# Kernel tuning notes

Hardware: AMD Instinct MI355X
Metric: run time of the kernel (lower is better)

The kernel has to match this reference:

```python
import jax, jax.numpy as jnp
import numpy as np

NUM_HEADS = 8

def _l2norm(t, eps=1e-12):
    # F.normalize(p=2, dim=-1) with eps clamp
    n = jnp.sqrt(jnp.sum(t * t, axis=-1, keepdims=True))
    return t / jnp.maximum(n, eps)

def setup_inputs() -> dict:
    key = jax.random.key(0)
    ks = jax.random.split(key, 4)
    B, N, C = 16, 3136, 768
    x = jax.random.normal(ks[0], (B, N, C), dtype=jnp.float32)
    W_qkv = jax.random.normal(ks[1], (C, 3 * C), dtype=jnp.float32) * (1.0 / np.sqrt(C))
    temp = jnp.ones((NUM_HEADS, 1, 1), dtype=jnp.float32)
    W_proj = jax.random.normal(ks[2], (C, C), dtype=jnp.float32) * (1.0 / np.sqrt(C))
    b_proj = jnp.zeros((C,), dtype=jnp.float32)
    return {"x": x, "W_qkv": W_qkv, "temp": temp, "W_proj": W_proj, "b_proj": b_proj}

def reference(x, W_qkv, temp, W_proj, b_proj):
    B, N, C = x.shape
    h = NUM_HEADS
    d = C // h
    qkv = (x @ W_qkv).reshape(B, N, 3, h, d)
    qkv = jnp.transpose(qkv, (2, 0, 3, 1, 4))  # [3,B,h,N,d]
    q, k, v = qkv[0], qkv[1], qkv[2]           # [B,h,N,d]
    # transpose to channel-major: [B,h,d,N]
    q = jnp.swapaxes(q, -2, -1)
    k = jnp.swapaxes(k, -2, -1)
    v = jnp.swapaxes(v, -2, -1)
    q = _l2norm(q)
    k = _l2norm(k)
    # attn = k @ q^T over token dim: [B,h,d,d]
    attn = jnp.einsum('bhcn,bhen->bhce', k, q)
    attn = attn * temp  # temp broadcasts [h,1,1]
    attn = jax.nn.softmax(attn, axis=-1)
    out = jnp.einsum('bhce,bhen->bhcn', attn, v)  # [B,h,d,N]
    out = jnp.transpose(out, (0, 3, 1, 2)).reshape(B, N, C)
    return out @ W_proj + b_proj
```

## Files before the change

kernel.cpp:

```cpp
#include <hip/hip_runtime.h>

using bf16x8 = __attribute__((ext_vector_type(8))) __bf16;
using f32x4  = __attribute__((ext_vector_type(4))) float;

#define AS1 __attribute__((address_space(1)))
#define AS3 __attribute__((address_space(3)))

#define SB()     __builtin_amdgcn_s_barrier()
#define LGKM0()  asm volatile("s_waitcnt lgkmcnt(0)")
#define VM0()    asm volatile("s_waitcnt vmcnt(0)")
#define SCHED0() __builtin_amdgcn_sched_barrier(0)

__device__ __forceinline__ unsigned short f2bf(float f) {
    unsigned int x = __float_as_uint(f);
    x += 0x7fffu + ((x >> 16) & 1u);
    return (unsigned short)(x >> 16);
}

__device__ __forceinline__ int xcd_remap(int orig, int nwg) {
    int q = nwg >> 3, r = nwg & 7;
    int xcd = orig & 7, lin = orig >> 3;
    return (xcd < r ? xcd * (q + 1) : r * (q + 1) + (xcd - r) * q) + lin;
}

__global__ void cvt_f32_bf16_kernel(const float4* __restrict__ in, ushort4* __restrict__ out, int n4) {
    int stride = gridDim.x * blockDim.x;
    for (int i = blockIdx.x * blockDim.x + threadIdx.x; i < n4; i += stride) {
        float4 v = in[i];
        ushort4 o;
        o.x = f2bf(v.x); o.y = f2bf(v.y); o.z = f2bf(v.z); o.w = f2bf(v.w);
        out[i] = o;
    }
}

__global__ void transpose_f32_bf16_kernel(const float* __restrict__ W, unsigned short* __restrict__ Wt,
                                          int K, int N) {
    __shared__ float tile[32][33];
    int n0 = blockIdx.x << 5, k0 = blockIdx.y << 5;
    int tx = threadIdx.x, ty = threadIdx.y;
#pragma unroll
    for (int i = 0; i < 32; i += 8)
        tile[ty + i][tx] = W[(size_t)(k0 + ty + i) * N + (n0 + tx)];
    __syncthreads();
#pragma unroll
    for (int i = 0; i < 32; i += 8)
        Wt[(size_t)(n0 + ty + i) * K + (k0 + tx)] = f2bf(tile[tx][ty + i]);
}

__device__ __forceinline__ bf16x8 lds_read_swz(const char* base, int row, int ks, int lane) {
    int kbyte = (ks << 6) + ((lane >> 4) << 4);
    int off = (row << 7) + (kbyte ^ ((row & 7) << 4));
    return *(const bf16x8*)(base + off);
}

__device__ __forceinline__ void stage256x64(const unsigned short* g, int ldaE, int Mcap,
                                            char* dst, int tid) {
#pragma unroll
    for (int r = 0; r < 4; ++r) {
        int i = (r << 9) + tid;
        int row = i >> 3, slot = i & 7;
        int rg = row < Mcap ? row : Mcap - 1;
        size_t srcb = (size_t)rg * ((size_t)ldaE << 1) + ((slot ^ (row & 7)) << 4);
        __builtin_amdgcn_global_load_lds(
            (AS1 unsigned int*)(unsigned long long)((const char*)g + srcb),
            (AS3 unsigned int*)(dst + (i << 4)), 16, 0, 0);
    }
}

template <int OUTMODE>
__global__ __launch_bounds__(512, 2)
void gemm256_8ph(const unsigned short* __restrict__ A, const unsigned short* __restrict__ Bt,
                 unsigned short* __restrict__ obf, float* __restrict__ of32,
                 const float* __restrict__ bias,
                 int K, int lda, int Nld, int nbx, int nmt, int Mrows,
                 long strideA, long strideB, long strideO) {
    __shared__ char smem[131072];
    int tid = threadIdx.x, lane = tid & 63, w = tid >> 6;
    int wm = w >> 2, wn = w & 3;
    int l15 = lane & 15;

    int wg = xcd_remap(blockIdx.x, gridDim.x);
    int bx = wg % nbx; int r1 = wg / nbx; int mt = r1 % nmt; int b = r1 / nmt;
    int m0 = mt << 8, n0 = bx << 8;
    int Mcap = Mrows - m0; if (Mcap > 256) Mcap = 256;
    const unsigned short* Ag = A + (long)b * strideA + (size_t)m0 * lda;
    const unsigned short* Bg = Bt + (long)b * strideB + (size_t)n0 * K;
    int nkt = K >> 6;

    f32x4 zz = {0.f, 0.f, 0.f, 0.f};
    f32x4 acc[8][4];
#pragma unroll
    for (int a = 0; a < 8; ++a)
#pragma unroll
        for (int c = 0; c < 4; ++c) acc[a][c] = zz;

    stage256x64(Ag, lda, Mcap, smem, tid);
    stage256x64(Bg, K, 256, smem + 32768, tid);
    VM0();
    SB(); SCHED0();

    for (int t = 0; t < nkt; ++t) {
        const char* Ab = smem + ((t & 1) << 16);
        const char* Bb = Ab + 32768;
        char* An = smem + (((t + 1) & 1) << 16);
        int arow = (wm << 7) + l15;
        int brow = (wn << 6) + l15;

        bf16x8 aF[4], aG[4], bL[4], bH[4];
#pragma unroll
        for (int f = 0; f < 4; ++f) aF[f] = lds_read_swz(Ab, arow + (f << 4), 0, lane);
#pragma unroll
        for (int f = 0; f < 4; ++f) bL[f] = lds_read_swz(Bb, brow + (f << 4), 0, lane);
        if (t + 1 < nkt) stage256x64(Ag + ((t + 1) << 6), lda, Mcap, An, tid);
        SB(); LGKM0(); SCHED0();
        __builtin_amdgcn_s_setprio(1);
#pragma unroll
        for (int fm = 0; fm < 4; ++fm)
#pragma unroll
            for (int fn = 0; fn < 4; ++fn)
                acc[fm][fn] = __builtin_amdgcn_mfma_f32_16x16x32_bf16(aF[fm], bL[fn], acc[fm][fn], 0, 0, 0);
        __builtin_amdgcn_s_setprio(0);
        SB(); SCHED0();
#pragma unroll
        for (int f = 0; f < 4; ++f) aG[f] = lds_read_swz(Ab, arow + 64 + (f << 4), 0, lane);
        if (t + 1 < nkt) stage256x64(Bg + ((t + 1) << 6), K, 256, An + 32768, tid);
        SB(); LGKM0(); SCHED0();
        __builtin_amdgcn_s_setprio(1);
#pragma unroll
        for (int fm = 0; fm < 4; ++fm)
#pragma unroll
            for (int fn = 0; fn < 4; ++fn)
                acc[fm + 4][fn] = __builtin_amdgcn_mfma_f32_16x16x32_bf16(aG[fm], bL[fn], acc[fm + 4][fn], 0, 0, 0);
        __builtin_amdgcn_s_setprio(0);
        SB(); SCHED0();
#pragma unroll
        for (int f = 0; f < 4; ++f) aF[f] = lds_read_swz(Ab, arow + (f << 4), 1, lane);
#pragma unroll
        for (int f = 0; f < 4; ++f) bH[f] = lds_read_swz(Bb, brow + (f << 4), 1, lane);
        SB(); LGKM0(); SCHED0();
        __builtin_amdgcn_s_setprio(1);
#pragma unroll
        for (int fm = 0; fm < 4; ++fm)
#pragma unroll
            for (int fn = 0; fn < 4; ++fn)
                acc[fm][fn] = __builtin_amdgcn_mfma_f32_16x16x32_bf16(aF[fm], bH[fn], acc[fm][fn], 0, 0, 0);
        __builtin_amdgcn_s_setprio(0);
        SB(); SCHED0();
#pragma unroll
        for (int f = 0; f < 4; ++f) aG[f] = lds_read_swz(Ab, arow + 64 + (f << 4), 1, lane);
        SB(); LGKM0(); SCHED0();
        __builtin_amdgcn_s_setprio(1);
#pragma unroll
        for (int fm = 0; fm < 4; ++fm)
#pragma unroll
            for (int fn = 0; fn < 4; ++fn)
                acc[fm + 4][fn] = __builtin_amdgcn_mfma_f32_16x16x32_bf16(aG[fm], bH[fn], acc[fm + 4][fn], 0, 0, 0);
        __builtin_amdgcn_s_setprio(0);
        if (t + 1 < nkt) VM0();
        SB(); SCHED0();
    }

    int rbase = m0 + (wm << 7) + ((lane >> 4) << 2);
    int cbase = n0 + (wn << 6) + l15;
    if (OUTMODE == 0) {
#pragma unroll
        for (int fm = 0; fm < 8; ++fm)
#pragma unroll
            for (int j = 0; j < 4; ++j) {
                size_t ro = (size_t)(rbase + (fm << 4) + j) * Nld;
#pragma unroll
                for (int fn = 0; fn < 4; ++fn)
                    obf[ro + cbase + (fn << 4)] = f2bf(acc[fm][fn][j]);
            }
    } else {
        float bv[4];
#pragma unroll
        for (int fn = 0; fn < 4; ++fn) bv[fn] = bias[cbase + (fn << 4)];
#pragma unroll
        for (int fm = 0; fm < 8; ++fm)
#pragma unroll
            for (int j = 0; j < 4; ++j) {
                int rr = rbase + (fm << 4) + j;
                if (rr < Mrows) {
                    size_t ro = (long)b * strideO + (size_t)rr * Nld;
#pragma unroll
                    for (int fn = 0; fn < 4; ++fn)
                        of32[ro + cbase + (fn << 4)] = acc[fm][fn][j] + bv[fn];
                }
            }
    }
}

__global__ __launch_bounds__(256)
void cov_mfma_kernel(const unsigned short* __restrict__ qkv, float* __restrict__ S,
                     float* __restrict__ qn2, float* __restrict__ kn2) {
    __shared__ unsigned short Kl[96 * 40];
    __shared__ unsigned short Ql[96 * 40];
    int bh = blockIdx.x;
    int b = bh >> 3, h = bh & 7;
    int tok0 = blockIdx.y * 448;
    int tid = threadIdx.x;
    int lane = tid & 63, w = tid >> 6;
    int wr = w & 1, wc = w >> 1;
    int rot = tid & 7;

    f32x4 zz = {0.f, 0.f, 0.f, 0.f};
    f32x4 acc[3][3];
#pragma unroll
    for (int a = 0; a < 3; ++a)
#pragma unroll
        for (int c = 0; c < 3; ++c) acc[a][c] = zz;
    float qn = 0.f, kn = 0.f;

    const uint4* qg = (const uint4*)qkv;

    for (int step = 0; step < 14; ++step) {
        int tokBase = b * 3136 + tok0 + (step << 5);
        __syncthreads();
#pragma unroll
        for (int r = 0; r < 3; ++r) {
            int idx = (r << 8) + tid;
            int isK = idx >= 384;
            int j = isK ? idx - 384 : idx;
            int tok = j / 12, c = j % 12;
            uint4 u = qg[(size_t)(tokBase + tok) * 288 + h * 12 + (isK ? 96 : 0) + c];
            unsigned short* dst = isK ? Kl : Ql;
            const unsigned short* us = (const unsigned short*)&u;
#pragma unroll
            for (int i = 0; i < 8; ++i) {
                int e = (i + rot) & 7;
                dst[(c * 8 + e) * 40 + tok] = us[e];
            }
        }
        __syncthreads();
        if (tid < 96) {
#pragma unroll
            for (int t = 0; t < 4; ++t) {
                bf16x8 v = *(const bf16x8*)((const char*)Ql + tid * 80 + (t << 4));
#pragma unroll
                for (int i = 0; i < 8; ++i) { float f = (float)v[i]; qn = fmaf(f, f, qn); }
            }
        } else if (tid >= 128 && tid < 224) {
            int c = tid - 128;
#pragma unroll
            for (int t = 0; t < 4; ++t) {
                bf16x8 v = *(const bf16x8*)((const char*)Kl + c * 80 + (t << 4));
#pragma unroll
                for (int i = 0; i < 8; ++i) { float f = (float)v[i]; kn = fmaf(f, f, kn); }
            }
        }
        int kbyte = (lane >> 4) << 4;
        bf16x8 af[3], bfv[3];
#pragma unroll
        for (int f = 0; f < 3; ++f)
            af[f] = *(const bf16x8*)((const char*)Kl + (wr * 48 + f * 16 + (lane & 15)) * 80 + kbyte);
#pragma unroll
        for (int f = 0; f < 3; ++f)
            bfv[f] = *(const bf16x8*)((const char*)Ql + (wc * 48 + f * 16 + (lane & 15)) * 80 + kbyte);
#pragma unroll
        for (int fm = 0; fm < 3; ++fm)
#pragma unroll
            for (int fn = 0; fn < 3; ++fn)
                acc[fm][fn] = __builtin_amdgcn_mfma_f32_16x16x32_bf16(af[fm], bfv[fn], acc[fm][fn], 0, 0, 0);
    }

    float* Sb = S + (size_t)bh * 9216;
    int rloc = wr * 48 + ((lane >> 4) << 2);
    int cloc = wc * 48 + (lane & 15);
#pragma unroll
    for (int fm = 0; fm < 3; ++fm)
#pragma unroll
        for (int fn = 0; fn < 3; ++fn)
#pragma unroll
            for (int j = 0; j < 4; ++j)
                atomicAdd(&Sb[(rloc + fm * 16 + j) * 96 + cloc + fn * 16], acc[fm][fn][j]);
    if (tid < 96) atomicAdd(&qn2[bh * 96 + tid], qn);
    if (tid >= 128 && tid < 224) atomicAdd(&kn2[bh * 96 + tid - 128], kn);
}

__global__ __launch_bounds__(128)
void softmax_kernel(const float* __restrict__ S, const float* __restrict__ qn2,
                    const float* __restrict__ kn2, const float* __restrict__ temp,
                    unsigned short* __restrict__ attnT) {
    int bh = blockIdx.x, h = bh & 7;
    __shared__ float Sl[96 * 97];
    __shared__ float qinv[96];
    int tid = threadIdx.x;
    const float* Sg = S + (size_t)bh * 9216;
    for (int i = tid; i < 9216; i += 128) Sl[(i / 96) * 97 + (i % 96)] = Sg[i];
    if (tid < 96) qinv[tid] = 1.f / fmaxf(sqrtf(qn2[bh * 96 + tid]), 1e-12f);
    __syncthreads();
    if (tid < 96) {
        int c = tid;
        float scale = (1.f / fmaxf(sqrtf(kn2[bh * 96 + c]), 1e-12f)) * temp[h];
        float* row = &Sl[c * 97];
        float mx = -3.4e38f;
        for (int e = 0; e < 96; ++e) {
            float v = row[e] * scale * qinv[e];
            row[e] = v;
            mx = fmaxf(mx, v);
        }
        float s = 0.f;
        for (int e = 0; e < 96; ++e) {
            float p = __expf(row[e] - mx);
            row[e] = p;
            s += p;
        }
        float inv = 1.f / s;
        unsigned short* ab = attnT + (size_t)bh * 9216;
        for (int e = 0; e < 96; ++e) ab[e * 96 + c] = f2bf(row[e] * inv);
    }
}

__global__ __launch_bounds__(256)
void attn_M_kernel(const unsigned short* __restrict__ attnT, const unsigned short* __restrict__ wprojt,
                   unsigned short* __restrict__ MT) {
    int bh = blockIdx.x >> 2, oc = blockIdx.x & 3;
    int b = bh >> 3, h = bh & 7;
    int tid = threadIdx.x, lane = tid & 63, w = tid >> 6;
    int o0 = oc * 192 + w * 48;
    const unsigned short* At = attnT + (size_t)bh * 9216;

    f32x4 zz = {0.f, 0.f, 0.f, 0.f};
    f32x4 acc[6][3];
#pragma unroll
    for (int f = 0; f < 6; ++f)
#pragma unroll
        for (int g = 0; g < 3; ++g) acc[f][g] = zz;

#pragma unroll
    for (int ks = 0; ks < 3; ++ks) {
        int koff = ks * 32 + ((lane >> 4) << 3);
        bf16x8 a[6], bb[3];
#pragma unroll
        for (int f = 0; f < 6; ++f)
            a[f] = *(const bf16x8*)(At + (size_t)(f * 16 + (lane & 15)) * 96 + koff);
#pragma unroll
        for (int g = 0; g < 3; ++g)
            bb[g] = *(const bf16x8*)(wprojt + (size_t)(o0 + g * 16 + (lane & 15)) * 768 + h * 96 + koff);
#pragma unroll
        for (int f = 0; f < 6; ++f)
#pragma unroll
            for (int g = 0; g < 3; ++g)
                acc[f][g] = __builtin_amdgcn_mfma_f32_16x16x32_bf16(a[f], bb[g], acc[f][g], 0, 0, 0);
    }

#pragma unroll
    for (int f = 0; f < 6; ++f)
#pragma unroll
        for (int g = 0; g < 3; ++g) {
            int e = f * 16 + ((lane >> 4) << 2);
            int o = o0 + g * 16 + (lane & 15);
            ushort4 pk;
            pk.x = f2bf(acc[f][g][0]); pk.y = f2bf(acc[f][g][1]);
            pk.z = f2bf(acc[f][g][2]); pk.w = f2bf(acc[f][g][3]);
            *(ushort4*)&MT[((size_t)b * 768 + o) * 768 + h * 96 + e] = pk;
        }
}

extern "C" void kernel_launch(void* const* d_in, const int* in_sizes, int n_in,
                              void* d_out, int out_size, void* d_ws, size_t ws_size,
                              hipStream_t stream) {
    const float* x     = (const float*)d_in[0];
    const float* Wqkv  = (const float*)d_in[1];
    const float* temp  = (const float*)d_in[2];
    const float* Wproj = (const float*)d_in[3];
    const float* bproj = (const float*)d_in[4];
    float* out = (float*)d_out;
    char* ws = (char*)d_ws;

    unsigned short* xbf    = (unsigned short*)(ws);
    unsigned short* qkvbf  = (unsigned short*)(ws + 77070336);
    unsigned short* wqkvt  = (unsigned short*)(ws + 308281344);
    unsigned short* wprojt = (unsigned short*)(ws + 311820288);
    float*          Sbuf   = (float*)        (ws + 312999936);
    float*          qn2    = (float*)        (ws + 317718528);
    float*          kn2    = (float*)        (ws + 317767680);
    unsigned short* attnT  = (unsigned short*)(ws + 317816832);
    unsigned short* MT     = xbf;

    hipMemsetAsync(Sbuf, 0, 4718592 + 49152 + 49152, stream);

    cvt_f32_bf16_kernel<<<2048, 256, 0, stream>>>((const float4*)x, (ushort4*)xbf, 38535168 / 4);
    transpose_f32_bf16_kernel<<<dim3(72, 24), dim3(32, 8), 0, stream>>>(Wqkv, wqkvt, 768, 2304);
    transpose_f32_bf16_kernel<<<dim3(24, 24), dim3(32, 8), 0, stream>>>(Wproj, wprojt, 768, 768);

    gemm256_8ph<0><<<196 * 9, 512, 0, stream>>>(xbf, wqkvt, qkvbf, nullptr, nullptr,
                                                768, 768, 2304, 9, 196, 50176, 0, 0, 0);
    cov_mfma_kernel<<<dim3(128, 7), 256, 0, stream>>>(qkvbf, Sbuf, qn2, kn2);
    softmax_kernel<<<128, 128, 0, stream>>>(Sbuf, qn2, kn2, temp, attnT);
    attn_M_kernel<<<512, 256, 0, stream>>>(attnT, wprojt, MT);
    gemm256_8ph<1><<<16 * 13 * 3, 512, 0, stream>>>(qkvbf + 1536, MT, nullptr, out, bproj,
                                                    768, 2304, 768, 3, 13, 3136,
                                                    7225344L, 589824L, 2408448L);
}
```

Before: 431.2 us.

## Switch GEMMs to 256x128 tiles with triple-buffered LDS and counted vmcnt waits

Both GEMMs move from 256x256 tiles with double buffering to 256x128 tiles with a three-stage LDS ring. Loads run two k-steps ahead and use a partial vmcnt wait, so global loads overlap compute instead of draining every iteration. The smaller tile doubles the grid and halves the per-wave accumulators. In exchange, B reuse per tile drops, A is loaded twice as often, and 144KB of LDS per block may limit occupancy to one block per CU despite the launch bounds of 2.

```diff
diff --git a/kernel.cpp b/kernel.cpp
--- a/kernel.cpp
+++ b/kernel.cpp
@@ -9,6 +9,7 @@
 #define SB()     __builtin_amdgcn_s_barrier()
 #define LGKM0()  asm volatile("s_waitcnt lgkmcnt(0)")
 #define VM0()    asm volatile("s_waitcnt vmcnt(0)")
+#define VM6()    asm volatile("s_waitcnt vmcnt(6)")
 #define SCHED0() __builtin_amdgcn_sched_barrier(0)
 
 __device__ __forceinline__ unsigned short f2bf(float f) {
@@ -53,8 +54,8 @@
     return *(const bf16x8*)(base + off);
 }
 
-__device__ __forceinline__ void stage256x64(const unsigned short* g, int ldaE, int Mcap,
-                                            char* dst, int tid) {
+__device__ __forceinline__ void stageA256(const unsigned short* g, int ldaE, int Mcap,
+                                          char* dst, int tid) {
 #pragma unroll
     for (int r = 0; r < 4; ++r) {
         int i = (r << 9) + tid;
@@ -66,105 +67,103 @@
             (AS3 unsigned int*)(dst + (i << 4)), 16, 0, 0);
     }
 }
+__device__ __forceinline__ void stageB128(const unsigned short* g, int ldbE, char* dst, int tid) {
+#pragma unroll
+    for (int r = 0; r < 2; ++r) {
+        int i = (r << 9) + tid;
+        int row = i >> 3, slot = i & 7;
+        size_t srcb = (size_t)row * ((size_t)ldbE << 1) + ((slot ^ (row & 7)) << 4);
+        __builtin_amdgcn_global_load_lds(
+            (AS1 unsigned int*)(unsigned long long)((const char*)g + srcb),
+            (AS3 unsigned int*)(dst + (i << 4)), 16, 0, 0);
+    }
+}
 
 template <int OUTMODE>
 __global__ __launch_bounds__(512, 2)
-void gemm256_8ph(const unsigned short* __restrict__ A, const unsigned short* __restrict__ Bt,
-                 unsigned short* __restrict__ obf, float* __restrict__ of32,
-                 const float* __restrict__ bias,
-                 int K, int lda, int Nld, int nbx, int nmt, int Mrows,
-                 long strideA, long strideB, long strideO) {
-    __shared__ char smem[131072];
+void gemm_cnt_kernel(const unsigned short* __restrict__ A, const unsigned short* __restrict__ Bt,
+                     unsigned short* __restrict__ obf, float* __restrict__ of32,
+                     const float* __restrict__ bias,
+                     int K, int lda, int Nld, int nbx, int nmt, int Mrows,
+                     long strideA, long strideB, long strideO) {
+    __shared__ char smem[147456];
     int tid = threadIdx.x, lane = tid & 63, w = tid >> 6;
-    int wm = w >> 2, wn = w & 3;
+    int wm = w >> 1, wn = w & 1;
     int l15 = lane & 15;
 
     int wg = xcd_remap(blockIdx.x, gridDim.x);
     int bx = wg % nbx; int r1 = wg / nbx; int mt = r1 % nmt; int b = r1 / nmt;
-    int m0 = mt << 8, n0 = bx << 8;
+    int m0 = mt << 8, n0 = bx << 7;
     int Mcap = Mrows - m0; if (Mcap > 256) Mcap = 256;
     const unsigned short* Ag = A + (long)b * strideA + (size_t)m0 * lda;
     const unsigned short* Bg = Bt + (long)b * strideB + (size_t)n0 * K;
     int nkt = K >> 6;
 
     f32x4 zz = {0.f, 0.f, 0.f, 0.f};
-    f32x4 acc[8][4];
-#pragma unroll
-    for (int a = 0; a < 8; ++a)
+    f32x4 acc[4][4];
+#pragma unroll
+    for (int a = 0; a < 4; ++a)
 #pragma unroll
         for (int c = 0; c < 4; ++c) acc[a][c] = zz;
 
-    stage256x64(Ag, lda, Mcap, smem, tid);
-    stage256x64(Bg, K, 256, smem + 32768, tid);
-    VM0();
+    stageA256(Ag, lda, Mcap, smem, tid);
+    stageB128(Bg, K, smem + 98304, tid);
+    if (nkt > 1) {
+        stageA256(Ag + 64, lda, Mcap, smem + 32768, tid);
+        stageB128(Bg + 64, K, smem + 98304 + 16384, tid);
+        VM6();
+    } else {
+        VM0();
+    }
     SB(); SCHED0();
 
+    int arow = (wm << 6) + l15;
+    int brow = (wn << 6) + l15;
+
     for (int t = 0; t < nkt; ++t) {
-        const char* Ab = smem + ((t & 1) << 16);
-        const char* Bb = Ab + 32768;
-        char* An = smem + (((t + 1) & 1) << 16);
-        int arow = (wm << 7) + l15;
-        int brow = (wn << 6) + l15;
-
-        bf16x8 aF[4], aG[4], bL[4], bH[4];
+        const char* Ab = smem + (t % 3) * 32768;
+        const char* Bb = smem + 98304 + (t % 3) * 16384;
+        char* An = smem + ((t + 2) % 3) * 32768;
+        char* Bn = smem + 98304 + ((t + 2) % 3) * 16384;
+
+        bf16x8 aF[4], bF[4];
 #pragma unroll
         for (int f = 0; f < 4; ++f) aF[f] = lds_read_swz(Ab, arow + (f << 4), 0, lane);
 #pragma unroll
-        for (int f = 0; f < 4; ++f) bL[f] = lds_read_swz(Bb, brow + (f << 4), 0, lane);
-        if (t + 1 < nkt) stage256x64(Ag + ((t + 1) << 6), lda, Mcap, An, tid);
+        for (int f = 0; f < 4; ++f) bF[f] = lds_read_swz(Bb, brow + (f << 4), 0, lane);
+        if (t + 2 < nkt) stageA256(Ag + ((t + 2) << 6), lda, Mcap, An, tid);
         SB(); LGKM0(); SCHED0();
         __builtin_amdgcn_s_setprio(1);
 #pragma unroll
         for (int fm = 0; fm < 4; ++fm)
 #pragma unroll
             for (int fn = 0; fn < 4; ++fn)
-                acc[fm][fn] = __builtin_amdgcn_mfma_f32_16x16x32_bf16(aF[fm], bL[fn], acc[fm][fn], 0, 0, 0);
+                acc[fm][fn] = __builtin_amdgcn_mfma_f32_16x16x32_bf16(aF[fm], bF[fn], acc[fm][fn], 0, 0, 0);
         __builtin_amdgcn_s_setprio(0);
         SB(); SCHED0();
 #pragma unroll
-        for (int f = 0; f < 4; ++f) aG[f] = lds_read_swz(Ab, arow + 64 + (f << 4), 0, lane);
-        if (t + 1 < nkt) stage256x64(Bg + ((t + 1) << 6), K, 256, An + 32768, tid);
+        for (int f = 0; f < 4; ++f) aF[f] = lds_read_swz(Ab, arow + (f << 4), 1, lane);
+#pragma unroll
+        for (int f = 0; f < 4; ++f) bF[f] = lds_read_swz(Bb, brow + (f << 4), 1, lane);
+        if (t + 2 < nkt) stageB128(Bg + ((t + 2) << 6), K, Bn, tid);
         SB(); LGKM0(); SCHED0();
         __builtin_amdgcn_s_setprio(1);
 #pragma unroll
         for (int fm = 0; fm < 4; ++fm)
 #pragma unroll
             for (int fn = 0; fn < 4; ++fn)
-                acc[fm + 4][fn] = __builtin_amdgcn_mfma_f32_16x16x32_bf16(aG[fm], bL[fn], acc[fm + 4][fn], 0, 0, 0);
+                acc[fm][fn] = __builtin_amdgcn_mfma_f32_16x16x32_bf16(aF[fm], bF[fn], acc[fm][fn], 0, 0, 0);
         __builtin_amdgcn_s_setprio(0);
+        if (t + 2 < nkt) VM6();
+        else if (t + 1 < nkt) VM0();
         SB(); SCHED0();
-#pragma unroll
-        for (int f = 0; f < 4; ++f) aF[f] = lds_read_swz(Ab, arow + (f << 4), 1, lane);
-#pragma unroll
-        for (int f = 0; f < 4; ++f) bH[f] = lds_read_swz(Bb, brow + (f << 4), 1, lane);
-        SB(); LGKM0(); SCHED0();
-        __builtin_amdgcn_s_setprio(1);
-#pragma unroll
-        for (int fm = 0; fm < 4; ++fm)
-#pragma unroll
-            for (int fn = 0; fn < 4; ++fn)
-                acc[fm][fn] = __builtin_amdgcn_mfma_f32_16x16x32_bf16(aF[fm], bH[fn], acc[fm][fn], 0, 0, 0);
-        __builtin_amdgcn_s_setprio(0);
-        SB(); SCHED0();
-#pragma unroll
-        for (int f = 0; f < 4; ++f) aG[f] = lds_read_swz(Ab, arow + 64 + (f << 4), 1, lane);
-        SB(); LGKM0(); SCHED0();
-        __builtin_amdgcn_s_setprio(1);
-#pragma unroll
-        for (int fm = 0; fm < 4; ++fm)
-#pragma unroll
-            for (int fn = 0; fn < 4; ++fn)
-                acc[fm + 4][fn] = __builtin_amdgcn_mfma_f32_16x16x32_bf16(aG[fm], bH[fn], acc[fm + 4][fn], 0, 0, 0);
-        __builtin_amdgcn_s_setprio(0);
-        if (t + 1 < nkt) VM0();
-        SB(); SCHED0();
-    }
-
-    int rbase = m0 + (wm << 7) + ((lane >> 4) << 2);
+    }
+
+    int rbase = m0 + (wm << 6) + ((lane >> 4) << 2);
     int cbase = n0 + (wn << 6) + l15;
     if (OUTMODE == 0) {
 #pragma unroll
-        for (int fm = 0; fm < 8; ++fm)
+        for (int fm = 0; fm < 4; ++fm)
 #pragma unroll
             for (int j = 0; j < 4; ++j) {
                 size_t ro = (size_t)(rbase + (fm << 4) + j) * Nld;
@@ -177,7 +176,7 @@
 #pragma unroll
         for (int fn = 0; fn < 4; ++fn) bv[fn] = bias[cbase + (fn << 4)];
 #pragma unroll
-        for (int fm = 0; fm < 8; ++fm)
+        for (int fm = 0; fm < 4; ++fm)
 #pragma unroll
             for (int j = 0; j < 4; ++j) {
                 int rr = rbase + (fm << 4) + j;
@@ -385,12 +384,12 @@
     transpose_f32_bf16_kernel<<<dim3(72, 24), dim3(32, 8), 0, stream>>>(Wqkv, wqkvt, 768, 2304);
     transpose_f32_bf16_kernel<<<dim3(24, 24), dim3(32, 8), 0, stream>>>(Wproj, wprojt, 768, 768);
 
-    gemm256_8ph<0><<<196 * 9, 512, 0, stream>>>(xbf, wqkvt, qkvbf, nullptr, nullptr,
-                                                768, 768, 2304, 9, 196, 50176, 0, 0, 0);
+    gemm_cnt_kernel<0><<<196 * 18, 512, 0, stream>>>(xbf, wqkvt, qkvbf, nullptr, nullptr,
+                                                     768, 768, 2304, 18, 196, 50176, 0, 0, 0);
     cov_mfma_kernel<<<dim3(128, 7), 256, 0, stream>>>(qkvbf, Sbuf, qn2, kn2);
     softmax_kernel<<<128, 128, 0, stream>>>(Sbuf, qn2, kn2, temp, attnT);
     attn_M_kernel<<<512, 256, 0, stream>>>(attnT, wprojt, MT);
-    gemm256_8ph<1><<<16 * 13 * 3, 512, 0, stream>>>(qkvbf + 1536, MT, nullptr, out, bproj,
-                                                    768, 2304, 768, 3, 13, 3136,
-                                                    7225344L, 589824L, 2408448L);
-}
+    gemm_cnt_kernel<1><<<16 * 13 * 6, 512, 0, stream>>>(qkvbf + 1536, MT, nullptr, out, bproj,
+                                                        768, 2304, 768, 6, 13, 3136,
+                                                        7225344L, 589824L, 2408448L);
+}
```

After: 457.9 us. 6.2% more time.

## Restage GEMM pipeline in half tiles and fuse prep and softmax kernels

Applied to the files above, without the earlier changes.

The bf16 GEMM now stages A and B tiles as 128-row and 64-row halves, with two K-steps per loop iteration. Each half's global-to-LDS load is issued between MFMA clusters, and a partial vmcnt wait lets loads stay in flight across barriers. The launch bound drops to one block per CU, and the bf16 output uses nontemporal stores. The input conversion, both weight transposes and the memset are merged into one prep kernel. Softmax is fused with the attn×Wproj kernel through LDS, which removes the attnT round trip and several launches, at the cost of computing each softmax four times.

```diff
diff --git a/kernel.cpp b/kernel.cpp
--- a/kernel.cpp
+++ b/kernel.cpp
@@ -7,9 +7,10 @@
 #define AS3 __attribute__((address_space(3)))
 
 #define SB()     __builtin_amdgcn_s_barrier()
+#define SCHED0() __builtin_amdgcn_sched_barrier(0)
 #define LGKM0()  asm volatile("s_waitcnt lgkmcnt(0)")
+#define VM6()    asm volatile("s_waitcnt vmcnt(6)")
 #define VM0()    asm volatile("s_waitcnt vmcnt(0)")
-#define SCHED0() __builtin_amdgcn_sched_barrier(0)
 
 __device__ __forceinline__ unsigned short f2bf(float f) {
     unsigned int x = __float_as_uint(f);
@@ -23,57 +24,102 @@
     return (xcd < r ? xcd * (q + 1) : r * (q + 1) + (xcd - r) * q) + lin;
 }
 
-__global__ void cvt_f32_bf16_kernel(const float4* __restrict__ in, ushort4* __restrict__ out, int n4) {
-    int stride = gridDim.x * blockDim.x;
-    for (int i = blockIdx.x * blockDim.x + threadIdx.x; i < n4; i += stride) {
-        float4 v = in[i];
-        ushort4 o;
-        o.x = f2bf(v.x); o.y = f2bf(v.y); o.z = f2bf(v.z); o.w = f2bf(v.w);
-        out[i] = o;
-    }
-}
-
-__global__ void transpose_f32_bf16_kernel(const float* __restrict__ W, unsigned short* __restrict__ Wt,
-                                          int K, int N) {
+__global__ __launch_bounds__(256)
+void prep_kernel(const float* __restrict__ x, ushort4* __restrict__ xbf,
+                 const float* __restrict__ Wqkv, unsigned short* __restrict__ wqkvt,
+                 const float* __restrict__ Wproj, unsigned short* __restrict__ wprojt,
+                 float4* __restrict__ zbase) {
     __shared__ float tile[32][33];
-    int n0 = blockIdx.x << 5, k0 = blockIdx.y << 5;
-    int tx = threadIdx.x, ty = threadIdx.y;
-#pragma unroll
-    for (int i = 0; i < 32; i += 8)
-        tile[ty + i][tx] = W[(size_t)(k0 + ty + i) * N + (n0 + tx)];
-    __syncthreads();
-#pragma unroll
-    for (int i = 0; i < 32; i += 8)
-        Wt[(size_t)(n0 + ty + i) * K + (k0 + tx)] = f2bf(tile[tx][ty + i]);
-}
-
-__device__ __forceinline__ bf16x8 lds_read_swz(const char* base, int row, int ks, int lane) {
-    int kbyte = (ks << 6) + ((lane >> 4) << 4);
-    int off = (row << 7) + (kbyte ^ ((row & 7) << 4));
-    return *(const bf16x8*)(base + off);
-}
-
-__device__ __forceinline__ void stage256x64(const unsigned short* g, int ldaE, int Mcap,
-                                            char* dst, int tid) {
-#pragma unroll
-    for (int r = 0; r < 4; ++r) {
+    int bid = blockIdx.x, tid = threadIdx.x;
+    if (bid < 2304) {
+        const float* W; unsigned short* Wt; int K = 768, N; int bx, by;
+        if (bid < 1728) { W = Wqkv; Wt = wqkvt; N = 2304; bx = bid % 72; by = bid / 72; }
+        else            { int t = bid - 1728; W = Wproj; Wt = wprojt; N = 768; bx = t % 24; by = t / 24; }
+        int n0 = bx << 5, k0 = by << 5;
+        int tx = tid & 31, ty = tid >> 5;
+#pragma unroll
+        for (int i = 0; i < 32; i += 8)
+            tile[ty + i][tx] = W[(size_t)(k0 + ty + i) * N + (n0 + tx)];
+        __syncthreads();
+#pragma unroll
+        for (int i = 0; i < 32; i += 8)
+            Wt[(size_t)(n0 + ty + i) * K + (k0 + tx)] = f2bf(tile[tx][ty + i]);
+    } else if (bid < 4352) {
+        int vb = bid - 2304;
+        const float4* in = (const float4*)x;
+        int n4 = 38535168 / 4;
+        int stride = 2048 * 256;
+        for (int i = vb * 256 + tid; i < n4; i += stride) {
+            float4 v = in[i];
+            ushort4 o;
+            o.x = f2bf(v.x); o.y = f2bf(v.y); o.z = f2bf(v.z); o.w = f2bf(v.w);
+            xbf[i] = o;
+        }
+    } else {
+        int z = bid - 4352;
+        float4 zz4 = {0.f, 0.f, 0.f, 0.f};
+        for (int i = z * 256 + tid; i < 301056; i += 294 * 256) zbase[i] = zz4;
+    }
+}
+
+__device__ __forceinline__ void stA8(const char* Asrc, int ldaB, int Mcap, int h,
+                                     char* dst, int tid) {
+#pragma unroll
+    for (int r = 0; r < 2; ++r) {
         int i = (r << 9) + tid;
-        int row = i >> 3, slot = i & 7;
-        int rg = row < Mcap ? row : Mcap - 1;
-        size_t srcb = (size_t)rg * ((size_t)ldaE << 1) + ((slot ^ (row & 7)) << 4);
+        int rho = i >> 3, s = i & 7;
+        int grow = ((rho >> 6) << 7) + (h << 6) + (rho & 63);
+        if (grow >= Mcap) grow = Mcap - 1;
         __builtin_amdgcn_global_load_lds(
-            (AS1 unsigned int*)(unsigned long long)((const char*)g + srcb),
+            (AS1 unsigned int*)(unsigned long long)(Asrc + (size_t)grow * ldaB + ((s ^ (rho & 7)) << 4)),
             (AS3 unsigned int*)(dst + (i << 4)), 16, 0, 0);
     }
 }
+__device__ __forceinline__ void stB8(const char* Bsrc, int ldbB, int h, char* dst, int tid) {
+#pragma unroll
+    for (int r = 0; r < 2; ++r) {
+        int i = (r << 9) + tid;
+        int rho = i >> 3, s = i & 7;
+        int grow = ((rho >> 5) << 6) + (h << 5) + (rho & 31);
+        __builtin_amdgcn_global_lds:
+        __builtin_amdgcn_global_load_lds(
+            (AS1 unsigned int*)(unsigned long long)(Bsrc + (size_t)grow * ldbB + ((s ^ (rho & 7)) << 4)),
+            (AS3 unsigned int*)(dst + (i << 4)), 16, 0, 0);
+    }
+}
+
+__device__ __forceinline__ bf16x8 rdA8(const char* smem, int buf, int rh, int wm,
+                                       int f, int ks, int lane) {
+    int rho = (wm << 6) + (f << 4) + (lane & 15);
+    int kb = ((ks << 2) + (lane >> 4)) << 4;
+    return *(const bf16x8*)(smem + (buf << 16) + (rh << 14) + rho * 128 + (kb ^ ((rho & 7) << 4)));
+}
+__device__ __forceinline__ bf16x8 rdB8(const char* smem, int buf, int ch, int wn,
+                                       int g, int ks, int lane) {
+    int rho = (wn << 5) + (g << 4) + (lane & 15);
+    int kb = ((ks << 2) + (lane >> 4)) << 4;
+    return *(const bf16x8*)(smem + (buf << 16) + 32768 + (ch << 14) + rho * 128 + (kb ^ ((rho & 7) << 4)));
+}
+
+#define CL16(MB, CB, BREG)                                                     \
+    __builtin_amdgcn_s_setprio(1);                                             \
+    _Pragma("unroll") for (int f_ = 0; f_ < 4; ++f_) {                         \
+        _Pragma("unroll") for (int g_ = 0; g_ < 2; ++g_) {                     \
+            acc[(MB) + f_][(CB) + g_] = __builtin_amdgcn_mfma_f32_16x16x32_bf16( \
+                aF[f_][0], BREG[g_][0], acc[(MB) + f_][(CB) + g_], 0, 0, 0);   \
+            acc[(MB) + f_][(CB) + g_] = __builtin_amdgcn_mfma_f32_16x16x32_bf16( \
+                aF[f_][1], BREG[g_][1], acc[(MB) + f_][(CB) + g_], 0, 0, 0);   \
+        }                                                                      \
+    }                                                                          \
+    __builtin_amdgcn_s_setprio(0);
 
 template <int OUTMODE>
-__global__ __launch_bounds__(512, 2)
-void gemm256_8ph(const unsigned short* __restrict__ A, const unsigned short* __restrict__ Bt,
-                 unsigned short* __restrict__ obf, float* __restrict__ of32,
-                 const float* __restrict__ bias,
-                 int K, int lda, int Nld, int nbx, int nmt, int Mrows,
-                 long strideA, long strideB, long strideO) {
+__global__ __launch_bounds__(512, 1)
+void gemm8ph_kernel(const unsigned short* __restrict__ A, const unsigned short* __restrict__ Bt,
+                    unsigned short* __restrict__ obf, float* __restrict__ of32,
+                    const float* __restrict__ bias,
+                    int K, int lda, int Nld, int nbx, int nmt, int Mrows,
+                    long strideA, long strideB, long strideO) {
     __shared__ char smem[131072];
     int tid = threadIdx.x, lane = tid & 63, w = tid >> 6;
     int wm = w >> 2, wn = w & 3;
@@ -83,9 +129,10 @@
     int bx = wg % nbx; int r1 = wg / nbx; int mt = r1 % nmt; int b = r1 / nmt;
     int m0 = mt << 8, n0 = bx << 8;
     int Mcap = Mrows - m0; if (Mcap > 256) Mcap = 256;
-    const unsigned short* Ag = A + (long)b * strideA + (size_t)m0 * lda;
-    const unsigned short* Bg = Bt + (long)b * strideB + (size_t)n0 * K;
-    int nkt = K >> 6;
+    const char* AgB = (const char*)(A + (long)b * strideA + (size_t)m0 * lda);
+    const char* BgB = (const char*)(Bt + (long)b * strideB + (size_t)n0 * K);
+    int ldaB = lda << 1, ldbB = K << 1;
+    int nkt = K >> 6, niter = nkt >> 1;
 
     f32x4 zz = {0.f, 0.f, 0.f, 0.f};
     f32x4 acc[8][4];
@@ -94,69 +141,82 @@
 #pragma unroll
         for (int c = 0; c < 4; ++c) acc[a][c] = zz;
 
-    stage256x64(Ag, lda, Mcap, smem, tid);
-    stage256x64(Bg, K, 256, smem + 32768, tid);
-    VM0();
+    stA8(AgB, ldaB, Mcap, 0, smem, tid);
+    stB8(BgB, ldbB, 0, smem + 32768, tid);
+    stB8(BgB, ldbB, 1, smem + 32768 + 16384, tid);
+    stA8(AgB, ldaB, Mcap, 1, smem + 16384, tid);
+    stA8(AgB + 128, ldaB, Mcap, 0, smem + 65536, tid);
+    stB8(BgB + 128, ldbB, 0, smem + 65536 + 32768, tid);
+    stB8(BgB + 128, ldbB, 1, smem + 65536 + 32768 + 16384, tid);
+    VM6();
     SB(); SCHED0();
 
-    for (int t = 0; t < nkt; ++t) {
-        const char* Ab = smem + ((t & 1) << 16);
-        const char* Bb = Ab + 32768;
-        char* An = smem + (((t + 1) & 1) << 16);
-        int arow = (wm << 7) + l15;
-        int brow = (wn << 6) + l15;
-
-        bf16x8 aF[4], aG[4], bL[4], bH[4];
-#pragma unroll
-        for (int f = 0; f < 4; ++f) aF[f] = lds_read_swz(Ab, arow + (f << 4), 0, lane);
-#pragma unroll
-        for (int f = 0; f < 4; ++f) bL[f] = lds_read_swz(Bb, brow + (f << 4), 0, lane);
-        if (t + 1 < nkt) stage256x64(Ag + ((t + 1) << 6), lda, Mcap, An, tid);
-        SB(); LGKM0(); SCHED0();
-        __builtin_amdgcn_s_setprio(1);
-#pragma unroll
-        for (int fm = 0; fm < 4; ++fm)
-#pragma unroll
-            for (int fn = 0; fn < 4; ++fn)
-                acc[fm][fn] = __builtin_amdgcn_mfma_f32_16x16x32_bf16(aF[fm], bL[fn], acc[fm][fn], 0, 0, 0);
-        __builtin_amdgcn_s_setprio(0);
-        SB(); SCHED0();
-#pragma unroll
-        for (int f = 0; f < 4; ++f) aG[f] = lds_read_swz(Ab, arow + 64 + (f << 4), 0, lane);
-        if (t + 1 < nkt) stage256x64(Bg + ((t + 1) << 6), K, 256, An + 32768, tid);
-        SB(); LGKM0(); SCHED0();
-        __builtin_amdgcn_s_setprio(1);
-#pragma unroll
-        for (int fm = 0; fm < 4; ++fm)
-#pragma unroll
-            for (int fn = 0; fn < 4; ++fn)
-                acc[fm + 4][fn] = __builtin_amdgcn_mfma_f32_16x16x32_bf16(aG[fm], bL[fn], acc[fm + 4][fn], 0, 0, 0);
-        __builtin_amdgcn_s_setprio(0);
-        SB(); SCHED0();
-#pragma unroll
-        for (int f = 0; f < 4; ++f) aF[f] = lds_read_swz(Ab, arow + (f << 4), 1, lane);
-#pragma unroll
-        for (int f = 0; f < 4; ++f) bH[f] = lds_read_swz(Bb, brow + (f << 4), 1, lane);
-        SB(); LGKM0(); SCHED0();
-        __builtin_amdgcn_s_setprio(1);
-#pragma unroll
-        for (int fm = 0; fm < 4; ++fm)
-#pragma unroll
-            for (int fn = 0; fn < 4; ++fn)
-                acc[fm][fn] = __builtin_amdgcn_mfma_f32_16x16x32_bf16(aF[fm], bH[fn], acc[fm][fn], 0, 0, 0);
-        __builtin_amdgcn_s_setprio(0);
-        SB(); SCHED0();
-#pragma unroll
-        for (int f = 0; f < 4; ++f) aG[f] = lds_read_swz(Ab, arow + 64 + (f << 4), 1, lane);
-        SB(); LGKM0(); SCHED0();
-        __builtin_amdgcn_s_setprio(1);
-#pragma unroll
-        for (int fm = 0; fm < 4; ++fm)
-#pragma unroll
-            for (int fn = 0; fn < 4; ++fn)
-                acc[fm + 4][fn] = __builtin_amdgcn_mfma_f32_16x16x32_bf16(aG[fm], bH[fn], acc[fm + 4][fn], 0, 0, 0);
-        __builtin_amdgcn_s_setprio(0);
-        if (t + 1 < nkt) VM0();
+    bf16x8 aF[4][2], b0[2][2], b1[2][2];
+
+    for (int i = 0; i < niter; ++i) {
+        bool more = (i + 1 < niter);
+        long kb1 = ((long)(2 * i + 1)) << 7;
+        long kb2 = ((long)(2 * i + 2)) << 7;
+        long kb3 = ((long)(2 * i + 3)) << 7;
+
+#pragma unroll
+        for (int f = 0; f < 4; ++f) { aF[f][0] = rdA8(smem, 0, 0, wm, f, 0, lane);
+                                      aF[f][1] = rdA8(smem, 0, 0, wm, f, 1, lane); }
+#pragma unroll
+        for (int g = 0; g < 2; ++g) { b0[g][0] = rdB8(smem, 0, 0, wn, g, 0, lane);
+                                      b0[g][1] = rdB8(smem, 0, 0, wn, g, 1, lane); }
+        stA8(AgB + kb1, ldaB, Mcap, 1, smem + 65536 + 16384, tid);
+        SB(); LGKM0(); SCHED0();
+        CL16(0, 0, b0);
+        SB(); SCHED0();
+#pragma unroll
+        for (int g = 0; g < 2; ++g) { b1[g][0] = rdB8(smem, 0, 1, wn, g, 0, lane);
+                                      b1[g][1] = rdB8(smem, 0, 1, wn, g, 1, lane); }
+        if (more) stA8(AgB + kb2, ldaB, Mcap, 0, smem, tid);
+        SB(); LGKM0(); SCHED0();
+        CL16(0, 2, b1);
+        SB(); SCHED0();
+#pragma unroll
+        for (int f = 0; f < 4; ++f) { aF[f][0] = rdA8(smem, 0, 1, wm, f, 0, lane);
+                                      aF[f][1] = rdA8(smem, 0, 1, wm, f, 1, lane); }
+        if (more) stB8(BgB + kb2, ldbB, 0, smem + 32768, tid);
+        SB(); LGKM0(); SCHED0();
+        CL16(4, 0, b0);
+        SB(); SCHED0();
+        if (more) stB8(BgB + kb2, ldbB, 1, smem + 32768 + 16384, tid);
+        SB(); SCHED0();
+        CL16(4, 2, b1);
+        if (more) { VM6(); } else { VM0(); }
+        SB(); SCHED0();
+
+#pragma unroll
+        for (int f = 0; f < 4; ++f) { aF[f][0] = rdA8(smem, 1, 0, wm, f, 0, lane);
+                                      aF[f][1] = rdA8(smem, 1, 0, wm, f, 1, lane); }
+#pragma unroll
+        for (int g = 0; g < 2; ++g) { b0[g][0] = rdB8(smem, 1, 0, wn, g, 0, lane);
+                                      b0[g][1] = rdB8(smem, 1, 0, wn, g, 1, lane); }
+        if (more) stA8(AgB + kb2, ldaB, Mcap, 1, smem + 16384, tid);
+        SB(); LGKM0(); SCHED0();
+        CL16(0, 0, b0);
+        SB(); SCHED0();
+#pragma unroll
+        for (int g = 0; g < 2; ++g) { b1[g][0] = rdB8(smem, 1, 1, wn, g, 0, lane);
+                                      b1[g][1] = rdB8(smem, 1, 1, wn, g, 1, lane); }
+        if (more) stA8(AgB + kb3, ldaB, Mcap, 0, smem + 65536, tid);
+        SB(); LGKM0(); SCHED0();
+        CL16(0, 2, b1);
+        SB(); SCHED0();
+#pragma unroll
+        for (int f = 0; f < 4; ++f) { aF[f][0] = rdA8(smem, 1, 1, wm, f, 0, lane);
+                                      aF[f][1] = rdA8(smem, 1, 1, wm, f, 1, lane); }
+        if (more) stB8(BgB + kb3, ldbB, 0, smem + 65536 + 32768, tid);
+        SB(); LGKM0(); SCHED0();
+        CL16(4, 0, b0);
+        SB(); SCHED0();
+        if (more) stB8(BgB + kb3, ldbB, 1, smem + 65536 + 32768 + 16384, tid);
+        SB(); SCHED0();
+        CL16(4, 2, b1);
+        if (more) VM6();
         SB(); SCHED0();
     }
 
@@ -170,7 +230,7 @@
                 size_t ro = (size_t)(rbase + (fm << 4) + j) * Nld;
 #pragma unroll
                 for (int fn = 0; fn < 4; ++fn)
-                    obf[ro + cbase + (fn << 4)] = f2bf(acc[fm][fn][j]);
+                    __builtin_nontemporal_store(f2bf(acc[fm][fn][j]), &obf[ro + cbase + (fn << 4)]);
             }
     } else {
         float bv[4];
@@ -278,16 +338,19 @@
     if (tid >= 128 && tid < 224) atomicAdd(&kn2[bh * 96 + tid - 128], kn);
 }
 
-__global__ __launch_bounds__(128)
-void softmax_kernel(const float* __restrict__ S, const float* __restrict__ qn2,
-                    const float* __restrict__ kn2, const float* __restrict__ temp,
-                    unsigned short* __restrict__ attnT) {
-    int bh = blockIdx.x, h = bh & 7;
+__global__ __launch_bounds__(256)
+void softmax_M_kernel(const float* __restrict__ S, const float* __restrict__ qn2,
+                      const float* __restrict__ kn2, const float* __restrict__ temp,
+                      const unsigned short* __restrict__ wprojt, unsigned short* __restrict__ MT) {
+    int bh = blockIdx.x >> 2, oc = blockIdx.x & 3;
+    int h = bh & 7, b = bh >> 3;
     __shared__ float Sl[96 * 97];
     __shared__ float qinv[96];
-    int tid = threadIdx.x;
+    __shared__ unsigned short At[96 * 96];
+    int tid = threadIdx.x, lane = tid & 63, w = tid >> 6;
+    int l15 = lane & 15;
     const float* Sg = S + (size_t)bh * 9216;
-    for (int i = tid; i < 9216; i += 128) Sl[(i / 96) * 97 + (i % 96)] = Sg[i];
+    for (int i = tid; i < 9216; i += 256) Sl[(i / 96) * 97 + (i % 96)] = Sg[i];
     if (tid < 96) qinv[tid] = 1.f / fmaxf(sqrtf(qn2[bh * 96 + tid]), 1e-12f);
     __syncthreads();
     if (tid < 96) {
@@ -307,50 +370,39 @@
             s += p;
         }
         float inv = 1.f / s;
-        unsigned short* ab = attnT + (size_t)bh * 9216;
-        for (int e = 0; e < 96; ++e) ab[e * 96 + c] = f2bf(row[e] * inv);
-    }
-}
-
-__global__ __launch_bounds__(256)
-void attn_M_kernel(const unsigned short* __restrict__ attnT, const unsigned short* __restrict__ wprojt,
-                   unsigned short* __restrict__ MT) {
-    int bh = blockIdx.x >> 2, oc = blockIdx.x & 3;
-    int b = bh >> 3, h = bh & 7;
-    int tid = threadIdx.x, lane = tid & 63, w = tid >> 6;
+        for (int e = 0; e < 96; ++e) At[e * 96 + c] = f2bf(row[e] * inv);
+    }
+    __syncthreads();
+
     int o0 = oc * 192 + w * 48;
-    const unsigned short* At = attnT + (size_t)bh * 9216;
-
     f32x4 zz = {0.f, 0.f, 0.f, 0.f};
     f32x4 acc[6][3];
 #pragma unroll
     for (int f = 0; f < 6; ++f)
 #pragma unroll
         for (int g = 0; g < 3; ++g) acc[f][g] = zz;
-
 #pragma unroll
     for (int ks = 0; ks < 3; ++ks) {
         int koff = ks * 32 + ((lane >> 4) << 3);
         bf16x8 a[6], bb[3];
 #pragma unroll
         for (int f = 0; f < 6; ++f)
-            a[f] = *(const bf16x8*)(At + (size_t)(f * 16 + (lane & 15)) * 96 + koff);
+            a[f] = *(const bf16x8*)(At + (f * 16 + l15) * 96 + koff);
 #pragma unroll
         for (int g = 0; g < 3; ++g)
-            bb[g] = *(const bf16x8*)(wprojt + (size_t)(o0 + g * 16 + (lane & 15)) * 768 + h * 96 + koff);
+            bb[g] = *(const bf16x8*)(wprojt + (size_t)(o0 + g * 16 + l15) * 768 + h * 96 + koff);
 #pragma unroll
         for (int f = 0; f < 6; ++f)
 #pragma unroll
             for (int g = 0; g < 3; ++g)
                 acc[f][g] = __builtin_amdgcn_mfma_f32_16x16x32_bf16(a[f], bb[g], acc[f][g], 0, 0, 0);
     }
-
 #pragma unroll
     for (int f = 0; f < 6; ++f)
 #pragma unroll
         for (int g = 0; g < 3; ++g) {
             int e = f * 16 + ((lane >> 4) << 2);
-            int o = o0 + g * 16 + (lane & 15);
+            int o = o0 + g * 16 + l15;
             ushort4 pk;
             pk.x = f2bf(acc[f][g][0]); pk.y = f2bf(acc[f][g][1]);
             pk.z = f2bf(acc[f][g][2]); pk.w = f2bf(acc[f][g][3]);
@@ -376,21 +428,16 @@
     float*          Sbuf   = (float*)        (ws + 312999936);
     float*          qn2    = (float*)        (ws + 317718528);
     float*          kn2    = (float*)        (ws + 317767680);
-    unsigned short* attnT  = (unsigned short*)(ws + 317816832);
     unsigned short* MT     = xbf;
 
-    hipMemsetAsync(Sbuf, 0, 4718592 + 49152 + 49152, stream);
-
-    cvt_f32_bf16_kernel<<<2048, 256, 0, stream>>>((const float4*)x, (ushort4*)xbf, 38535168 / 4);
-    transpose_f32_bf16_kernel<<<dim3(72, 24), dim3(32, 8), 0, stream>>>(Wqkv, wqkvt, 768, 2304);
-    transpose_f32_bf16_kernel<<<dim3(24, 24), dim3(32, 8), 0, stream>>>(Wproj, wprojt, 768, 768);
-
-    gemm256_8ph<0><<<196 * 9, 512, 0, stream>>>(xbf, wqkvt, qkvbf, nullptr, nullptr,
-                                                768, 768, 2304, 9, 196, 50176, 0, 0, 0);
+    prep_kernel<<<4646, 256, 0, stream>>>(x, (ushort4*)xbf, Wqkv, wqkvt, Wproj, wprojt,
+                                          (float4*)Sbuf);
+
+    gemm8ph_kernel<0><<<196 * 9, 512, 0, stream>>>(xbf, wqkvt, qkvbf, nullptr, nullptr,
+                                                   768, 768, 2304, 9, 196, 50176, 0, 0, 0);
     cov_mfma_kernel<<<dim3(128, 7), 256, 0, stream>>>(qkvbf, Sbuf, qn2, kn2);
-    softmax_kernel<<<128, 128, 0, stream>>>(Sbuf, qn2, kn2, temp, attnT);
-    attn_M_kernel<<<512, 256, 0, stream>>>(attnT, wprojt, MT);
-    gemm256_8ph<1><<<16 * 13 * 3, 512, 0, stream>>>(qkvbf + 1536, MT, nullptr, out, bproj,
-                                                    768, 2304, 768, 3, 13, 3136,
-                                                    7225344L, 589824L, 2408448L);
-}
+    softmax_M_kernel<<<512, 256, 0, stream>>>(Sbuf, qn2, kn2, temp, wprojt, MT);
+    gemm8ph_kernel<1><<<16 * 13 * 3, 512, 0, stream>>>(qkvbf + 1536, MT, nullptr, out, bproj,
+                                                       768, 2304, 768, 3, 13, 3136,
+                                                       7225344L, 589824L, 2408448L);
+}
```

Result: faster. 400.7 us (-7.1%).
